# Performance work log

Measured on AMD Instinct MI355X. Metric: run time of the kernel, lower is better.

The kernel has to match this reference:

```python
import jax, jax.numpy as jnp
import numpy as np

NUM_PATCHES = 4
PATCH_RADIUS = 0.2


def setup_inputs() -> dict:
    key = jax.random.key(0)
    points = jax.random.normal(key, (64, 65536, 6), dtype=jnp.float32)
    return {"points": points}


def _fps(xyz, n_samples):
    """Furthest point sampling (pointnet2 convention: start at index 0).
    xyz: (B, N, 3) -> (B, n_samples) int32 indices."""
    B, N, _ = xyz.shape

    def body(carry, _):
        min_d, last_idx = carry                                   # (B,N), (B,)
        last = jnp.take_along_axis(xyz, last_idx[:, None, None], axis=1)  # (B,1,3)
        d = jnp.sum((xyz - last) ** 2, axis=-1)                   # (B,N)
        min_d = jnp.minimum(min_d, d)
        nxt = jnp.argmax(min_d, axis=1).astype(jnp.int32)
        return (min_d, nxt), last_idx

    init = (jnp.full((B, N), 1e10, dtype=xyz.dtype),
            jnp.zeros((B,), dtype=jnp.int32))
    (_, _), idxs = jax.lax.scan(body, init, None, length=n_samples)
    return idxs.T                                                  # (B, n_samples)


def reference(points):
    B, N, C = points.shape
    xyz = points[..., :3]

    # 1) pick patch centers via FPS
    centers_idx = _fps(xyz, NUM_PATCHES)                           # (B,P)
    centers = jnp.take_along_axis(xyz, centers_idx[..., None], axis=1)  # (B,P,3)

    # 2) distance of every point to nearest center -> drop mask
    dist = jnp.linalg.norm(xyz[:, :, None, :] - centers[:, None, :, :], axis=-1)  # (B,N,P)
    min_dist = jnp.min(dist, axis=2)                               # (B,N)
    keep = min_dist >= PATCH_RADIUS                                # (B,N) bool, True = kept

    # 3) stable compaction: kept points first (original order preserved),
    #    then repeat-fill pattern valid_points[j % num_valid]
    order = jnp.argsort(jnp.logical_not(keep).astype(jnp.int32), axis=1, stable=True)  # (B,N)
    num_valid = jnp.sum(keep, axis=1)                              # (B,)
    j = jnp.arange(N, dtype=jnp.int32)[None, :]                    # (1,N)
    k = j % jnp.maximum(num_valid, 1)[:, None]                     # (B,N)
    src = jnp.take_along_axis(order, k, axis=1)                    # (B,N)
    out = jnp.take_along_axis(points, src[..., None], axis=1)      # (B,N,C)

    # all points dropped -> zeros (matches torch branch)
    return jnp.where((num_valid > 0)[:, None, None], out, jnp.zeros_like(out))
```

## Files before the change

### kernel.cpp

```cpp
#include <hip/hip_runtime.h>
#include <stdint.h>

#define NN 65536
#define BB 64
#define TPB 256

#define FBPB 32
#define FGRID (BB * FBPB)
#define FPPB 2048
#define FLPT 8

#define GBPB 16
#define GGRID (BB * GBPB)
#define GLPT 16

__device__ __forceinline__ float sqdist(float x, float y, float z,
                                        float cx, float cy, float cz) {
    float dx = __fsub_rn(x, cx);
    float dy = __fsub_rn(y, cy);
    float dz = __fsub_rn(z, cz);
    return __fadd_rn(__fadd_rn(__fmul_rn(dx, dx), __fmul_rn(dy, dy)),
                     __fmul_rn(dz, dz));
}

__device__ __forceinline__ unsigned long long pack_key(float v, int i) {
    return ((unsigned long long)__float_as_uint(v) << 32) |
           (unsigned long long)(0xFFFFFFFFu - (unsigned)i);
}

__device__ __forceinline__ int key_idx(unsigned long long key) {
    return (int)(0xFFFFFFFFu - (unsigned)(key & 0xFFFFFFFFu));
}

__device__ __forceinline__ int reduce_part(const unsigned long long* partKey,
                                           int a, int b) {
    const unsigned long long* s = partKey + a * FGRID + b * FBPB;
    unsigned long long bk = s[0];
    #pragma unroll
    for (int w = 1; w < FBPB; ++w) bk = (s[w] > bk) ? s[w] : bk;
    return key_idx(bk);
}

template<int NC>
__global__ __launch_bounds__(TPB) void fps_pass(
        const float* __restrict__ pts, unsigned long long* partKey) {
    const int gb = blockIdx.x;
    const int b = gb >> 5, blk = gb & 31;
    const int tid = threadIdx.x;
    const int lane = tid & 63, wid = tid >> 6;
    const float* base = pts + (size_t)b * NN * 6;

    float cx[NC], cy[NC], cz[NC];
    cx[0] = base[0]; cy[0] = base[1]; cz[0] = base[2];
    #pragma unroll
    for (int k = 1; k < NC; ++k) {
        int idx = reduce_part(partKey, k - 1, b);
        const float* p = base + (size_t)idx * 6;
        cx[k] = p[0]; cy[k] = p[1]; cz[k] = p[2];
    }

    float bestv = -1.0f; int besti = 0x7fffffff;
    #pragma unroll
    for (int l = 0; l < FLPT; ++l) {
        const int p = blk * FPPB + l * TPB + tid;
        const float* q = base + (size_t)p * 6;
        float2 xy = *(const float2*)q;
        float  zz = q[2];
        float d = sqdist(xy.x, xy.y, zz, cx[0], cy[0], cz[0]);
        #pragma unroll
        for (int k = 1; k < NC; ++k)
            d = fminf(d, sqdist(xy.x, xy.y, zz, cx[k], cy[k], cz[k]));
        if (d > bestv) { bestv = d; besti = p; }
    }
    unsigned long long key = pack_key(bestv, besti);
    #pragma unroll
    for (int off = 32; off > 0; off >>= 1) {
        unsigned long long ok = __shfl_down(key, off, 64);
        if (ok > key) key = ok;
    }
    __shared__ unsigned long long s_k[4];
    if (lane == 0) s_k[wid] = key;
    __syncthreads();
    if (tid == 0) {
        unsigned long long bk = s_k[0];
        #pragma unroll
        for (int w = 1; w < 4; ++w) bk = (s_k[w] > bk) ? s_k[w] : bk;
        partKey[(NC - 1) * FGRID + gb] = bk;
    }
}

__global__ __launch_bounds__(TPB) void fps_final(
        const float* __restrict__ pts,
        const unsigned long long* __restrict__ partKey,
        uint64_t* __restrict__ masks) {
    const int gb = blockIdx.x;
    const int b = gb >> 5, blk = gb & 31;
    const int tid = threadIdx.x;
    const int lane = tid & 63, wid = tid >> 6;
    const float* base = pts + (size_t)b * NN * 6;

    float cx[4], cy[4], cz[4];
    cx[0] = base[0]; cy[0] = base[1]; cz[0] = base[2];
    #pragma unroll
    for (int k = 1; k < 4; ++k) {
        int idx = reduce_part(partKey, k - 1, b);
        const float* p = base + (size_t)idx * 6;
        cx[k] = p[0]; cy[k] = p[1]; cz[k] = p[2];
    }
    uint64_t* mb = masks + (size_t)b * 1024;

    #pragma unroll
    for (int l = 0; l < FLPT; ++l) {
        const int p = blk * FPPB + l * TPB + tid;
        const float* q = base + (size_t)p * 6;
        float2 xy = *(const float2*)q;
        float  zz = q[2];
        float d = sqdist(xy.x, xy.y, zz, cx[0], cy[0], cz[0]);
        #pragma unroll
        for (int k = 1; k < 4; ++k)
            d = fminf(d, sqdist(xy.x, xy.y, zz, cx[k], cy[k], cz[k]));
        int keep = (__fsqrt_rn(d) >= 0.2f) ? 1 : 0;
        uint64_t m = __ballot(keep);
        if (lane == 0) mb[blk * 32 + l * 4 + wid] = m;
    }
}

__global__ __launch_bounds__(TPB) void gather_kernel(
        const float* __restrict__ pts, const uint64_t* __restrict__ masks,
        float* __restrict__ out) {
    const int gb = blockIdx.x;
    const int b = gb >> 4, blk = gb & 15;
    const int tid = threadIdx.x;
    const int lane = tid & 63, wid = tid >> 6;
    __shared__ uint64_t s_m[1024];
    __shared__ int s_pre[1024];
    __shared__ int s_ws[4], s_wo[4];
    __shared__ int s_nv;

    const uint64_t* mb = masks + (size_t)b * 1024;
    uint64_t w[4];
    int cnt = 0;
    #pragma unroll
    for (int k = 0; k < 4; ++k) {
        w[k] = mb[tid * 4 + k];
        s_m[tid * 4 + k] = w[k];
        cnt += __popcll(w[k]);
    }
    int incl = cnt;
    #pragma unroll
    for (int off = 1; off < 64; off <<= 1) {
        int v = __shfl_up(incl, off, 64);
        if (lane >= off) incl += v;
    }
    if (lane == 63) s_ws[wid] = incl;
    __syncthreads();
    if (tid == 0) {
        int run = 0;
        #pragma unroll
        for (int q = 0; q < 4; ++q) { s_wo[q] = run; run += s_ws[q]; }
        s_nv = run;
    }
    __syncthreads();
    int run = s_wo[wid] + incl - cnt;
    #pragma unroll
    for (int k = 0; k < 4; ++k) {
        s_pre[tid * 4 + k] = run;
        run += __popcll(w[k]);
    }
    __syncthreads();

    const int nv = s_nv;
    const float* baseP = pts + (size_t)b * NN * 6;
    float* ob = out + (size_t)b * NN * 6;

    if (nv <= 0) {
        float2 zz = make_float2(0.f, 0.f);
        #pragma unroll
        for (int l = 0; l < GLPT; ++l) {
            int j = blk * 4096 + l * TPB + tid;
            float2* o = (float2*)(ob + (size_t)j * 6);
            o[0] = zz; o[1] = zz; o[2] = zz;
        }
        return;
    }

    #pragma unroll
    for (int l = 0; l < GLPT; ++l) {
        int j = blk * 4096 + l * TPB + tid;
        int jj = (int)((unsigned)j % (unsigned)nv);
        int wd = 0;
        #pragma unroll
        for (int s = 512; s > 0; s >>= 1) {
            int cand = wd + s;
            if (cand < 1024 && s_pre[cand] <= jj) wd = cand;
        }
        int r = jj - s_pre[wd];
        uint64_t m = s_m[wd];
        int bit = 0;
        int c = __popcll(m & 0xFFFFFFFFull);
        if (r >= c) { r -= c; m >>= 32; bit += 32; }
        c = __popcll(m & 0xFFFFull);
        if (r >= c) { r -= c; m >>= 16; bit += 16; }
        c = __popcll(m & 0xFFull);
        if (r >= c) { r -= c; m >>= 8; bit += 8; }
        c = __popcll(m & 0xFull);
        if (r >= c) { r -= c; m >>= 4; bit += 4; }
        c = __popcll(m & 0x3ull);
        if (r >= c) { r -= c; m >>= 2; bit += 2; }
        if (r >= (int)(m & 1ull)) { bit += 1; }
        int src = wd * 64 + bit;
        const float2* p = (const float2*)(baseP + (size_t)src * 6);
        float2* o = (float2*)(ob + (size_t)j * 6);
        float2 r0 = p[0], r1 = p[1], r2 = p[2];
        o[0] = r0; o[1] = r1; o[2] = r2;
    }
}

extern "C" void kernel_launch(void* const* d_in, const int* in_sizes, int n_in,
                              void* d_out, int out_size, void* d_ws, size_t ws_size,
                              hipStream_t stream) {
    const float* pts = (const float*)d_in[0];
    float* out = (float*)d_out;

    unsigned long long* partKey = (unsigned long long*)d_ws;
    uint64_t* masks = (uint64_t*)((char*)d_ws + (64 << 10));

    fps_pass<1><<<FGRID, TPB, 0, stream>>>(pts, partKey);
    fps_pass<2><<<FGRID, TPB, 0, stream>>>(pts, partKey);
    fps_pass<3><<<FGRID, TPB, 0, stream>>>(pts, partKey);
    fps_final<<<FGRID, TPB, 0, stream>>>(pts, partKey, masks);
    gather_kernel<<<GGRID, TPB, 0, stream>>>(pts, masks, out);
}
```

Baseline: 247.0 us.

## Fuse FPS passes, mask and gather into one kernel with per-batch spin barriers

Replaces the five kernel launches with a single kernel. Each block keeps its 4096 points' xyz and running min distances in registers across the four FPS phases and syncs with the other blocks of its batch through atomic counters and flags. This avoids re-reading the point cloud once per pass and removes launch gaps. The cost is a per-batch inter-block barrier that depends on all 16 blocks of a batch being co-resident (1024 blocks with launch_bounds(256,4)), plus a memset and extra register pressure.

```diff
diff --git a/kernel.cpp b/kernel.cpp
--- a/kernel.cpp
+++ b/kernel.cpp
@@ -4,15 +4,10 @@
 #define NN 65536
 #define BB 64
 #define TPB 256
-
-#define FBPB 32
-#define FGRID (BB * FBPB)
-#define FPPB 2048
-#define FLPT 8
-
-#define GBPB 16
-#define GGRID (BB * GBPB)
-#define GLPT 16
+#define BPB 16
+#define GRID (BB * BPB)
+#define PPT 16
+#define PPBK 4096
 
 __device__ __forceinline__ float sqdist(float x, float y, float z,
                                         float cx, float cy, float cz) {
@@ -27,126 +22,127 @@
     return ((unsigned long long)__float_as_uint(v) << 32) |
            (unsigned long long)(0xFFFFFFFFu - (unsigned)i);
 }
-
 __device__ __forceinline__ int key_idx(unsigned long long key) {
     return (int)(0xFFFFFFFFu - (unsigned)(key & 0xFFFFFFFFu));
 }
 
-__device__ __forceinline__ int reduce_part(const unsigned long long* partKey,
-                                           int a, int b) {
-    const unsigned long long* s = partKey + a * FGRID + b * FBPB;
-    unsigned long long bk = s[0];
-    #pragma unroll
-    for (int w = 1; w < FBPB; ++w) bk = (s[w] > bk) ? s[w] : bk;
-    return key_idx(bk);
-}
-
-template<int NC>
-__global__ __launch_bounds__(TPB) void fps_pass(
-        const float* __restrict__ pts, unsigned long long* partKey) {
-    const int gb = blockIdx.x;
-    const int b = gb >> 5, blk = gb & 31;
-    const int tid = threadIdx.x;
-    const int lane = tid & 63, wid = tid >> 6;
-    const float* base = pts + (size_t)b * NN * 6;
-
-    float cx[NC], cy[NC], cz[NC];
-    cx[0] = base[0]; cy[0] = base[1]; cz[0] = base[2];
-    #pragma unroll
-    for (int k = 1; k < NC; ++k) {
-        int idx = reduce_part(partKey, k - 1, b);
-        const float* p = base + (size_t)idx * 6;
-        cx[k] = p[0]; cy[k] = p[1]; cz[k] = p[2];
-    }
-
-    float bestv = -1.0f; int besti = 0x7fffffff;
-    #pragma unroll
-    for (int l = 0; l < FLPT; ++l) {
-        const int p = blk * FPPB + l * TPB + tid;
-        const float* q = base + (size_t)p * 6;
-        float2 xy = *(const float2*)q;
-        float  zz = q[2];
-        float d = sqdist(xy.x, xy.y, zz, cx[0], cy[0], cz[0]);
-        #pragma unroll
-        for (int k = 1; k < NC; ++k)
-            d = fminf(d, sqdist(xy.x, xy.y, zz, cx[k], cy[k], cz[k]));
-        if (d > bestv) { bestv = d; besti = p; }
-    }
-    unsigned long long key = pack_key(bestv, besti);
-    #pragma unroll
-    for (int off = 32; off > 0; off >>= 1) {
-        unsigned long long ok = __shfl_down(key, off, 64);
-        if (ok > key) key = ok;
-    }
-    __shared__ unsigned long long s_k[4];
-    if (lane == 0) s_k[wid] = key;
-    __syncthreads();
-    if (tid == 0) {
-        unsigned long long bk = s_k[0];
-        #pragma unroll
-        for (int w = 1; w < 4; ++w) bk = (s_k[w] > bk) ? s_k[w] : bk;
-        partKey[(NC - 1) * FGRID + gb] = bk;
-    }
-}
-
-__global__ __launch_bounds__(TPB) void fps_final(
+__global__ __launch_bounds__(TPB, 4) void fused_kernel(
         const float* __restrict__ pts,
-        const unsigned long long* __restrict__ partKey,
-        uint64_t* __restrict__ masks) {
-    const int gb = blockIdx.x;
-    const int b = gb >> 5, blk = gb & 31;
-    const int tid = threadIdx.x;
-    const int lane = tid & 63, wid = tid >> 6;
-    const float* base = pts + (size_t)b * NN * 6;
-
-    float cx[4], cy[4], cz[4];
-    cx[0] = base[0]; cy[0] = base[1]; cz[0] = base[2];
-    #pragma unroll
-    for (int k = 1; k < 4; ++k) {
-        int idx = reduce_part(partKey, k - 1, b);
-        const float* p = base + (size_t)idx * 6;
-        cx[k] = p[0]; cy[k] = p[1]; cz[k] = p[2];
-    }
-    uint64_t* mb = masks + (size_t)b * 1024;
-
-    #pragma unroll
-    for (int l = 0; l < FLPT; ++l) {
-        const int p = blk * FPPB + l * TPB + tid;
-        const float* q = base + (size_t)p * 6;
-        float2 xy = *(const float2*)q;
-        float  zz = q[2];
-        float d = sqdist(xy.x, xy.y, zz, cx[0], cy[0], cz[0]);
-        #pragma unroll
-        for (int k = 1; k < 4; ++k)
-            d = fminf(d, sqdist(xy.x, xy.y, zz, cx[k], cy[k], cz[k]));
-        int keep = (__fsqrt_rn(d) >= 0.2f) ? 1 : 0;
-        uint64_t m = __ballot(keep);
-        if (lane == 0) mb[blk * 32 + l * 4 + wid] = m;
-    }
-}
-
-__global__ __launch_bounds__(TPB) void gather_kernel(
-        const float* __restrict__ pts, const uint64_t* __restrict__ masks,
+        unsigned long long* flag,
+        int* cnt,
+        unsigned long long* partKey,
+        unsigned long long* masks,
         float* __restrict__ out) {
     const int gb = blockIdx.x;
     const int b = gb >> 4, blk = gb & 15;
     const int tid = threadIdx.x;
     const int lane = tid & 63, wid = tid >> 6;
+    const float* base = pts + (size_t)b * NN * 6;
+
+    float x[PPT], y[PPT], z[PPT], mind[PPT];
+    #pragma unroll
+    for (int l = 0; l < PPT; ++l) {
+        const int p = blk * PPBK + l * TPB + tid;
+        const float* q = base + (size_t)p * 6;
+        float2 xy = *(const float2*)q;
+        x[l] = xy.x; y[l] = xy.y; z[l] = q[2];
+        mind[l] = 1e10f;
+    }
+    float cx = base[0], cy = base[1], cz = base[2];
+
+    __shared__ unsigned long long s_k[4];
+    __shared__ float s_ctr[3];
+
+    for (int ph = 0; ph < 4; ++ph) {
+        float bestv = -1.0f; int besti = 0;
+        #pragma unroll
+        for (int l = 0; l < PPT; ++l) {
+            float d = sqdist(x[l], y[l], z[l], cx, cy, cz);
+            float m = fminf(mind[l], d);
+            mind[l] = m;
+            if (m > bestv) { bestv = m; besti = blk * PPBK + l * TPB + tid; }
+        }
+        if (ph == 3) break;
+
+        unsigned long long key = pack_key(bestv, besti);
+        #pragma unroll
+        for (int off = 32; off > 0; off >>= 1) {
+            unsigned long long ok = __shfl_down(key, off, 64);
+            if (ok > key) key = ok;
+        }
+        if (lane == 0) s_k[wid] = key;
+        __syncthreads();
+        if (tid == 0) {
+            unsigned long long bk = s_k[0];
+            #pragma unroll
+            for (int w = 1; w < 4; ++w) bk = (s_k[w] > bk) ? s_k[w] : bk;
+            __hip_atomic_store(&partKey[ph * GRID + gb], bk,
+                               __ATOMIC_RELEASE, __HIP_MEMORY_SCOPE_AGENT);
+            int prev = atomicAdd(&cnt[ph * BB + b], 1);
+            unsigned long long win;
+            if (prev == BPB - 1) {
+                const unsigned long long* s = partKey + ph * GRID + b * BPB;
+                win = __hip_atomic_load(&s[0], __ATOMIC_ACQUIRE,
+                                        __HIP_MEMORY_SCOPE_AGENT);
+                #pragma unroll
+                for (int w = 1; w < BPB; ++w) {
+                    unsigned long long v = __hip_atomic_load(
+                        &s[w], __ATOMIC_ACQUIRE, __HIP_MEMORY_SCOPE_AGENT);
+                    if (v > win) win = v;
+                }
+                __hip_atomic_store(&flag[ph * BB + b], win,
+                                   __ATOMIC_RELEASE, __HIP_MEMORY_SCOPE_AGENT);
+            } else {
+                do {
+                    win = __hip_atomic_load(&flag[ph * BB + b],
+                                            __ATOMIC_ACQUIRE,
+                                            __HIP_MEMORY_SCOPE_AGENT);
+                    if (!win) __builtin_amdgcn_s_sleep(8);
+                } while (!win);
+            }
+            const float* c = base + (size_t)key_idx(win) * 6;
+            s_ctr[0] = c[0]; s_ctr[1] = c[1]; s_ctr[2] = c[2];
+        }
+        __syncthreads();
+        cx = s_ctr[0]; cy = s_ctr[1]; cz = s_ctr[2];
+    }
+
+    unsigned long long* mb = masks + (size_t)b * 1024;
+    #pragma unroll
+    for (int l = 0; l < PPT; ++l) {
+        int keep = (__fsqrt_rn(mind[l]) >= 0.2f) ? 1 : 0;
+        unsigned long long m = __ballot(keep);
+        if (lane == 0)
+            __hip_atomic_store(&mb[blk * 64 + l * 4 + wid], m,
+                               __ATOMIC_RELAXED, __HIP_MEMORY_SCOPE_AGENT);
+    }
+    __threadfence();
+    __syncthreads();
+    if (tid == 0) {
+        atomicAdd(&cnt[3 * BB + b], 1);
+        int c;
+        do {
+            c = __hip_atomic_load(&cnt[3 * BB + b], __ATOMIC_ACQUIRE,
+                                  __HIP_MEMORY_SCOPE_AGENT);
+            if (c < BPB) __builtin_amdgcn_s_sleep(8);
+        } while (c < BPB);
+    }
+    __syncthreads();
+
     __shared__ uint64_t s_m[1024];
     __shared__ int s_pre[1024];
     __shared__ int s_ws[4], s_wo[4];
-    __shared__ int s_nv;
-
-    const uint64_t* mb = masks + (size_t)b * 1024;
+    __shared__ int s_nvs;
     uint64_t w[4];
-    int cnt = 0;
+    int cnt4 = 0;
     #pragma unroll
     for (int k = 0; k < 4; ++k) {
-        w[k] = mb[tid * 4 + k];
+        w[k] = __hip_atomic_load(&mb[tid * 4 + k], __ATOMIC_RELAXED,
+                                 __HIP_MEMORY_SCOPE_AGENT);
         s_m[tid * 4 + k] = w[k];
-        cnt += __popcll(w[k]);
-    }
-    int incl = cnt;
+        cnt4 += __popcll(w[k]);
+    }
+    int incl = cnt4;
     #pragma unroll
     for (int off = 1; off < 64; off <<= 1) {
         int v = __shfl_up(incl, off, 64);
@@ -158,10 +154,10 @@
         int run = 0;
         #pragma unroll
         for (int q = 0; q < 4; ++q) { s_wo[q] = run; run += s_ws[q]; }
-        s_nv = run;
-    }
-    __syncthreads();
-    int run = s_wo[wid] + incl - cnt;
+        s_nvs = run;
+    }
+    __syncthreads();
+    int run = s_wo[wid] + incl - cnt4;
     #pragma unroll
     for (int k = 0; k < 4; ++k) {
         s_pre[tid * 4 + k] = run;
@@ -169,24 +165,21 @@
     }
     __syncthreads();
 
-    const int nv = s_nv;
-    const float* baseP = pts + (size_t)b * NN * 6;
+    const int nv = s_nvs;
     float* ob = out + (size_t)b * NN * 6;
-
     if (nv <= 0) {
         float2 zz = make_float2(0.f, 0.f);
         #pragma unroll
-        for (int l = 0; l < GLPT; ++l) {
-            int j = blk * 4096 + l * TPB + tid;
+        for (int l = 0; l < PPT; ++l) {
+            int j = blk * PPBK + l * TPB + tid;
             float2* o = (float2*)(ob + (size_t)j * 6);
             o[0] = zz; o[1] = zz; o[2] = zz;
         }
         return;
     }
-
-    #pragma unroll
-    for (int l = 0; l < GLPT; ++l) {
-        int j = blk * 4096 + l * TPB + tid;
+    #pragma unroll
+    for (int l = 0; l < PPT; ++l) {
+        int j = blk * PPBK + l * TPB + tid;
         int jj = (int)((unsigned)j % (unsigned)nv);
         int wd = 0;
         #pragma unroll
@@ -196,8 +189,8 @@
         }
         int r = jj - s_pre[wd];
         uint64_t m = s_m[wd];
-        int bit = 0;
-        int c = __popcll(m & 0xFFFFFFFFull);
+        int bit = 0, c;
+        c = __popcll(m & 0xFFFFFFFFull);
         if (r >= c) { r -= c; m >>= 32; bit += 32; }
         c = __popcll(m & 0xFFFFull);
         if (r >= c) { r -= c; m >>= 16; bit += 16; }
@@ -209,7 +202,7 @@
         if (r >= c) { r -= c; m >>= 2; bit += 2; }
         if (r >= (int)(m & 1ull)) { bit += 1; }
         int src = wd * 64 + bit;
-        const float2* p = (const float2*)(baseP + (size_t)src * 6);
+        const float2* p = (const float2*)(base + (size_t)src * 6);
         float2* o = (float2*)(ob + (size_t)j * 6);
         float2 r0 = p[0], r1 = p[1], r2 = p[2];
         o[0] = r0; o[1] = r1; o[2] = r2;
@@ -222,12 +215,11 @@
     const float* pts = (const float*)d_in[0];
     float* out = (float*)d_out;
 
-    unsigned long long* partKey = (unsigned long long*)d_ws;
-    uint64_t* masks = (uint64_t*)((char*)d_ws + (64 << 10));
-
-    fps_pass<1><<<FGRID, TPB, 0, stream>>>(pts, partKey);
-    fps_pass<2><<<FGRID, TPB, 0, stream>>>(pts, partKey);
-    fps_pass<3><<<FGRID, TPB, 0, stream>>>(pts, partKey);
-    fps_final<<<FGRID, TPB, 0, stream>>>(pts, partKey, masks);
-    gather_kernel<<<GGRID, TPB, 0, stream>>>(pts, masks, out);
-}
+    unsigned long long* flag    = (unsigned long long*)d_ws;
+    int*                cnt     = (int*)((char*)d_ws + 2048);
+    unsigned long long* partKey = (unsigned long long*)((char*)d_ws + 4096);
+    unsigned long long* masks   = (unsigned long long*)((char*)d_ws + (64 << 10));
+
+    hipMemsetAsync(d_ws, 0, 4096, stream);
+    fused_kernel<<<GRID, TPB, 0, stream>>>(pts, flag, cnt, partKey, masks, out);
+}
```

Result: slower. 747.9 us (+202.8%).
